# Optimization experiments

Hardware: AMD Instinct MI355X
Metric: run time of the kernel (lower is better)

Reference implementation:

```python
import jax, jax.numpy as jnp
import numpy as np


def setup_inputs() -> dict:
    key = jax.random.key(0)
    k1, k2, k3 = jax.random.split(key, 3)
    B, N, F = 32, 1024, 128
    x = jax.random.normal(k1, (B, N, F), dtype=jnp.float32)
    adj = jax.random.uniform(k2, (B, N, N), dtype=jnp.float32)
    # Linear(in_feature=128, out_feature=128) params (Kaiming-ish scale)
    W = jax.random.normal(k3, (F, F), dtype=jnp.float32) * (1.0 / np.sqrt(F))
    b = jnp.zeros((F,), dtype=jnp.float32)
    return {"x": x, "adj": adj, "W": W, "b": b}


def reference(x, adj, W, b):
    # h = W(x) ; dropout is identity in inference mode
    h = jnp.einsum("bnf,fg->bng", x, W) + b          # [B,N,F]
    h = jnp.einsum("bnm,bmf->bnf", adj, h)           # neighbor aggregation
    return jax.nn.relu(h + x)                          # residual + ReLU
```

## Files before the change

kernel.cpp:

```cpp
#include <hip/hip_runtime.h>
#include <stdint.h>

typedef unsigned short u16;
typedef __attribute__((ext_vector_type(4))) u16    u16x4;
typedef __attribute__((ext_vector_type(8))) u16    u16x8;
typedef __attribute__((ext_vector_type(4))) float  f32x4;
typedef __attribute__((ext_vector_type(8))) __bf16 bf16x8;

__device__ __forceinline__ u16 f2bf(float f) {
    union { float f; uint32_t u; } v; v.f = f;
    uint32_t u = v.u;
    uint32_t rb = 0x7FFFu + ((u >> 16) & 1u);
    return (u16)((u + rb) >> 16);
}

__device__ __forceinline__ bf16x8 cvt8(f32x4 a, f32x4 b) {
    bf16x8 r;
    r[0] = (__bf16)a.x; r[1] = (__bf16)a.y; r[2] = (__bf16)a.z; r[3] = (__bf16)a.w;
    r[4] = (__bf16)b.x; r[5] = (__bf16)b.y; r[6] = (__bf16)b.z; r[7] = (__bf16)b.w;
    return r;
}

__global__ __launch_bounds__(256) void gcn_wt(const float* __restrict__ W,
                                              u16* __restrict__ Wt) {
    int idx = blockIdx.x * 256 + threadIdx.x;
    int k = idx >> 7, f = idx & 127;
    Wt[f * 128 + k] = f2bf(W[idx]);
}

__global__ __launch_bounds__(256) void gcn_xw(const float* __restrict__ x,
                                              const u16* __restrict__ Wt,
                                              const float* __restrict__ bias,
                                              u16* __restrict__ hT) {
    __shared__ u16 Wl[128 * 128];
    __shared__ u16 Xl[128 * 128];
    const int t  = threadIdx.x;
    const int bb = blockIdx.x >> 3;
    const int n0 = (blockIdx.x & 7) << 7;

#pragma unroll
    for (int i = 0; i < 16; ++i) {
        int o  = i * 256 + t;
        int f  = o >> 5;
        int kb = (o & 31) * 8;
        u16x4 v = *(const u16x4*)((const char*)Wt + o * 8);
        *(u16x4*)((char*)Wl + f * 256 + (kb ^ ((f & 7) << 4))) = v;
    }
    const float* xb = x + (size_t)bb * (1024 * 128) + (size_t)n0 * 128;
#pragma unroll
    for (int i = 0; i < 16; ++i) {
        int o4 = i * 256 + t;
        int n  = o4 >> 5;
        int kb = (o4 & 31) * 8;
        f32x4 v = *(const f32x4*)(xb + (size_t)o4 * 4);
        u16x4 h; h.x = f2bf(v.x); h.y = f2bf(v.y); h.z = f2bf(v.z); h.w = f2bf(v.w);
        *(u16x4*)((char*)Xl + n * 256 + (kb ^ ((n & 7) << 4))) = h;
    }
    __syncthreads();

    const int w = t >> 6, l = t & 63;
    const int wr = w >> 1, wc = w & 1;
    f32x4 acc[4][4] = {};
#pragma unroll
    for (int kk = 0; kk < 4; ++kk) {
        const int kbyte = kk * 64 + (l >> 4) * 16;
        bf16x8 a[4], b[4];
#pragma unroll
        for (int mf = 0; mf < 4; ++mf) {
            int fl = wr * 64 + mf * 16 + (l & 15);
            a[mf] = *(const bf16x8*)((const char*)Wl + fl * 256 + (kbyte ^ ((fl & 7) << 4)));
        }
#pragma unroll
        for (int nn = 0; nn < 4; ++nn) {
            int nl = wc * 64 + nn * 16 + (l & 15);
            b[nn] = *(const bf16x8*)((const char*)Xl + nl * 256 + (kbyte ^ ((nl & 7) << 4)));
        }
#pragma unroll
        for (int mf = 0; mf < 4; ++mf)
#pragma unroll
            for (int nn = 0; nn < 4; ++nn)
                acc[mf][nn] = __builtin_amdgcn_mfma_f32_16x16x32_bf16(
                    a[mf], b[nn], acc[mf][nn], 0, 0, 0);
    }

    u16* ho = hT + (size_t)bb * 131072;
#pragma unroll
    for (int mf = 0; mf < 4; ++mf) {
        int fbase = wr * 64 + mf * 16 + (l >> 4) * 4;
#pragma unroll
        for (int r = 0; r < 4; ++r) {
            float bv = bias[fbase + r];
#pragma unroll
            for (int nn = 0; nn < 4; ++nn) {
                int n = wc * 64 + nn * 16 + (l & 15);
                ho[(size_t)(fbase + r) * 1024 + n0 + n] = f2bf(acc[mf][nn][r] + bv);
            }
        }
    }
}

__global__ __launch_bounds__(256) void gcn_agg(const float* __restrict__ adj,
                                               const u16* __restrict__ hT,
                                               const float* __restrict__ x,
                                               float* __restrict__ out) {
    __shared__ float Al[2][64 * 64];
    __shared__ u16   Bl[2][128 * 64];

    const int t = threadIdx.x;
    const int L  = (blockIdx.x & 7) * 64 + (blockIdx.x >> 3);
    const int bb = L >> 4;
    const int r0 = (L & 15) << 6;

    const float* adjb = adj + (size_t)bb * 1048576 + (size_t)r0 * 1024;
    const u16*   hTb  = hT + (size_t)bb * 131072;

    const int w = t >> 6, l = t & 63;
    const int wr = w >> 1, wc = w & 1;

    const float* srcA[4];
    const u16*   srcB[4];
#pragma unroll
    for (int i = 0; i < 4; ++i) {
        int c  = (w * 4 + i) * 64 + l;
        int rA = c >> 4, cbA = ((c & 15) * 16) ^ ((rA & 7) << 4);
        srcA[i] = adjb + (size_t)rA * 1024 + (cbA >> 2);
        int fB = c >> 3, cbB = ((c & 7) * 16) ^ ((fB & 7) << 4);
        srcB[i] = hTb + (size_t)fB * 1024 + (cbB >> 1);
    }

#define STAGE(buf, ks)                                                          \
    do {                                                                        \
        const int k0 = (ks) * 64;                                               \
        _Pragma("unroll")                                                       \
        for (int i = 0; i < 4; ++i) {                                           \
            __builtin_amdgcn_global_load_lds(                                   \
                (const __attribute__((address_space(1))) void*)(srcA[i] + k0),  \
                (__attribute__((address_space(3))) void*)((char*)&Al[buf][0] + (w * 4 + i) * 1024), \
                16, 0, 0);                                                      \
            __builtin_amdgcn_global_load_lds(                                   \
                (const __attribute__((address_space(1))) void*)(srcB[i] + k0),  \
                (__attribute__((address_space(3))) void*)((char*)&Bl[buf][0] + (w * 4 + i) * 1024), \
                16, 0, 0);                                                      \
        }                                                                       \
    } while (0)

#define COMPUTE(buf)                                                            \
    do {                                                                        \
        _Pragma("unroll")                                                       \
        for (int kk = 0; kk < 2; ++kk) {                                        \
            const int ke = kk * 32 + (l >> 4) * 8;                              \
            bf16x8 a[2], b[4];                                                  \
            _Pragma("unroll")                                                   \
            for (int mf = 0; mf < 2; ++mf) {                                    \
                int rl  = wr * 32 + mf * 16 + (l & 15);                         \
                int cb0 = (ke * 4) ^ ((rl & 7) << 4);                           \
                int cb1 = (ke * 4 + 16) ^ ((rl & 7) << 4);                      \
                f32x4 lo = *(const f32x4*)((const char*)&Al[buf][0] + rl * 256 + cb0); \
                f32x4 hi = *(const f32x4*)((const char*)&Al[buf][0] + rl * 256 + cb1); \
                a[mf] = cvt8(lo, hi);                                           \
            }                                                                   \
            _Pragma("unroll")                                                   \
            for (int nn = 0; nn < 4; ++nn) {                                    \
                int fl = wc * 64 + nn * 16 + (l & 15);                          \
                int cb = (ke * 2) ^ ((fl & 7) << 4);                            \
                b[nn] = *(const bf16x8*)((const char*)&Bl[buf][0] + fl * 128 + cb); \
            }                                                                   \
            _Pragma("unroll")                                                   \
            for (int mf = 0; mf < 2; ++mf)                                      \
                _Pragma("unroll")                                               \
                for (int nn = 0; nn < 4; ++nn)                                  \
                    acc[mf][nn] = __builtin_amdgcn_mfma_f32_16x16x32_bf16(      \
                        a[mf], b[nn], acc[mf][nn], 0, 0, 0);                    \
        }                                                                       \
    } while (0)

    f32x4 acc[2][4] = {};

    STAGE(0, 0);
    __syncthreads();
    for (int ks = 0; ks < 16; ks += 2) {
        STAGE(1, ks + 1);
        COMPUTE(0);
        __syncthreads();
        if (ks + 2 < 16) STAGE(0, ks + 2);
        COMPUTE(1);
        __syncthreads();
    }
#undef STAGE
#undef COMPUTE

    const float* xb = x + (size_t)bb * 131072;
    float*       ob = out + (size_t)bb * 131072;
#pragma unroll
    for (int mf = 0; mf < 2; ++mf) {
#pragma unroll
        for (int j = 0; j < 4; ++j) {
            int r = r0 + wr * 32 + mf * 16 + (l >> 4) * 4 + j;
#pragma unroll
            for (int nn = 0; nn < 4; ++nn) {
                int f = wc * 64 + nn * 16 + (l & 15);
                size_t idx = (size_t)r * 128 + f;
                float v = acc[mf][nn][j] + xb[idx];
                ob[idx] = fmaxf(v, 0.0f);
            }
        }
    }
}

extern "C" void kernel_launch(void* const* d_in, const int* in_sizes, int n_in,
                              void* d_out, int out_size, void* d_ws, size_t ws_size,
                              hipStream_t stream) {
    const float* x    = (const float*)d_in[0];
    const float* adj  = (const float*)d_in[1];
    const float* W    = (const float*)d_in[2];
    const float* bias = (const float*)d_in[3];
    float* out = (float*)d_out;

    u16* hT = (u16*)d_ws;
    u16* Wt = (u16*)((char*)d_ws + (size_t)32 * 131072 * 2);

    gcn_wt <<<dim3(64),  dim3(256), 0, stream>>>(W, Wt);
    gcn_xw <<<dim3(256), dim3(256), 0, stream>>>(x, Wt, bias, hT);
    gcn_agg<<<dim3(512), dim3(256), 0, stream>>>(adj, hT, x, out);
}
```

Measured before the change: 44.96 us.

## Stage adjacency through registers, convert to bf16 before LDS, use 512-thread blocks

The aggregation kernel no longer uses direct global-to-LDS async loads. Each thread now loads fp32 adj and bf16 hT into registers two k-steps ahead, converts adj to bf16 once, and writes it into a swizzled bf16 LDS tile. This halves LDS footprint and LDS read traffic for A and removes the repeated per-wave fp32-to-bf16 conversion. Blocks grow to 512 threads (8 waves, 16 rows each) with a custom waitcnt+barrier. The trade-off is more register pressure, manual rounding work per thread, and extra VGPR-to-LDS write instructions.

```diff
diff --git a/kernel.cpp b/kernel.cpp
--- a/kernel.cpp
+++ b/kernel.cpp
@@ -12,13 +12,6 @@
     uint32_t u = v.u;
     uint32_t rb = 0x7FFFu + ((u >> 16) & 1u);
     return (u16)((u + rb) >> 16);
-}
-
-__device__ __forceinline__ bf16x8 cvt8(f32x4 a, f32x4 b) {
-    bf16x8 r;
-    r[0] = (__bf16)a.x; r[1] = (__bf16)a.y; r[2] = (__bf16)a.z; r[3] = (__bf16)a.w;
-    r[4] = (__bf16)b.x; r[5] = (__bf16)b.y; r[6] = (__bf16)b.z; r[7] = (__bf16)b.w;
-    return r;
 }
 
 __global__ __launch_bounds__(256) void gcn_wt(const float* __restrict__ W,
@@ -99,12 +92,12 @@
     }
 }
 
-__global__ __launch_bounds__(256) void gcn_agg(const float* __restrict__ adj,
-                                               const u16* __restrict__ hT,
-                                               const float* __restrict__ x,
-                                               float* __restrict__ out) {
-    __shared__ float Al[2][64 * 64];
-    __shared__ u16   Bl[2][128 * 64];
+__global__ __launch_bounds__(512, 4) void gcn_agg(const float* __restrict__ adj,
+                                                  const u16* __restrict__ hT,
+                                                  const float* __restrict__ x,
+                                                  float* __restrict__ out) {
+    __shared__ u16 Al[2][64 * 64];
+    __shared__ u16 Bl[2][128 * 64];
 
     const int t = threadIdx.x;
     const int L  = (blockIdx.x & 7) * 64 + (blockIdx.x >> 3);
@@ -117,92 +110,92 @@
     const int w = t >> 6, l = t & 63;
     const int wr = w >> 1, wc = w & 1;
 
-    const float* srcA[4];
-    const u16*   srcB[4];
-#pragma unroll
-    for (int i = 0; i < 4; ++i) {
-        int c  = (w * 4 + i) * 64 + l;
-        int rA = c >> 4, cbA = ((c & 15) * 16) ^ ((rA & 7) << 4);
-        srcA[i] = adjb + (size_t)rA * 1024 + (cbA >> 2);
-        int fB = c >> 3, cbB = ((c & 7) * 16) ^ ((fB & 7) << 4);
-        srcB[i] = hTb + (size_t)fB * 1024 + (cbB >> 1);
-    }
-
-#define STAGE(buf, ks)                                                          \
-    do {                                                                        \
-        const int k0 = (ks) * 64;                                               \
-        _Pragma("unroll")                                                       \
-        for (int i = 0; i < 4; ++i) {                                           \
-            __builtin_amdgcn_global_load_lds(                                   \
-                (const __attribute__((address_space(1))) void*)(srcA[i] + k0),  \
-                (__attribute__((address_space(3))) void*)((char*)&Al[buf][0] + (w * 4 + i) * 1024), \
-                16, 0, 0);                                                      \
-            __builtin_amdgcn_global_load_lds(                                   \
-                (const __attribute__((address_space(1))) void*)(srcB[i] + k0),  \
-                (__attribute__((address_space(3))) void*)((char*)&Bl[buf][0] + (w * 4 + i) * 1024), \
-                16, 0, 0);                                                      \
-        }                                                                       \
+    const int rA  = t >> 3, k8 = t & 7;
+    const float* gA  = adjb + (size_t)rA * 1024 + k8 * 8;
+    const u16*   gB0 = hTb + (size_t)rA * 1024 + k8 * 8;
+    const u16*   gB1 = gB0 + 64 * 1024;
+    const int ldsA  = rA * 128 + ((k8 * 16) ^ ((rA & 7) << 4));
+    const int ldsB0 = rA * 128 + ((k8 * 16) ^ ((rA & 7) << 4));
+    const int ldsB1 = (64 + rA) * 128 + ((k8 * 16) ^ ((rA & 7) << 4));
+
+#define LOADT(ar, br, ks)                                   \
+    do {                                                    \
+        const int k0 = (ks) * 64;                           \
+        ar[0] = *(const f32x4*)(gA + k0);                   \
+        ar[1] = *(const f32x4*)(gA + k0 + 4);               \
+        br[0] = *(const u16x8*)(gB0 + k0);                  \
+        br[1] = *(const u16x8*)(gB1 + k0);                  \
     } while (0)
+
+#define WRITET(buf, ar, br)                                 \
+    do {                                                    \
+        u16x8 ha;                                           \
+        ha[0] = f2bf(ar[0].x); ha[1] = f2bf(ar[0].y);       \
+        ha[2] = f2bf(ar[0].z); ha[3] = f2bf(ar[0].w);       \
+        ha[4] = f2bf(ar[1].x); ha[5] = f2bf(ar[1].y);       \
+        ha[6] = f2bf(ar[1].z); ha[7] = f2bf(ar[1].w);       \
+        *(u16x8*)((char*)&Al[buf][0] + ldsA)  = ha;         \
+        *(u16x8*)((char*)&Bl[buf][0] + ldsB0) = br[0];      \
+        *(u16x8*)((char*)&Bl[buf][0] + ldsB1) = br[1];      \
+    } while (0)
+
+#define BARRIER() asm volatile("s_waitcnt lgkmcnt(0)\ns_barrier" ::: "memory")
 
 #define COMPUTE(buf)                                                            \
     do {                                                                        \
         _Pragma("unroll")                                                       \
         for (int kk = 0; kk < 2; ++kk) {                                        \
-            const int ke = kk * 32 + (l >> 4) * 8;                              \
-            bf16x8 a[2], b[4];                                                  \
-            _Pragma("unroll")                                                   \
-            for (int mf = 0; mf < 2; ++mf) {                                    \
-                int rl  = wr * 32 + mf * 16 + (l & 15);                         \
-                int cb0 = (ke * 4) ^ ((rl & 7) << 4);                           \
-                int cb1 = (ke * 4 + 16) ^ ((rl & 7) << 4);                      \
-                f32x4 lo = *(const f32x4*)((const char*)&Al[buf][0] + rl * 256 + cb0); \
-                f32x4 hi = *(const f32x4*)((const char*)&Al[buf][0] + rl * 256 + cb1); \
-                a[mf] = cvt8(lo, hi);                                           \
-            }                                                                   \
+            const int kbyte = kk * 64 + (l >> 4) * 16;                          \
+            const int rl = wr * 16 + (l & 15);                                  \
+            bf16x8 a = *(const bf16x8*)((const char*)&Al[buf][0] + rl * 128 +   \
+                                        (kbyte ^ ((rl & 7) << 4)));             \
+            bf16x8 b[4];                                                        \
             _Pragma("unroll")                                                   \
             for (int nn = 0; nn < 4; ++nn) {                                    \
                 int fl = wc * 64 + nn * 16 + (l & 15);                          \
-                int cb = (ke * 2) ^ ((fl & 7) << 4);                            \
-                b[nn] = *(const bf16x8*)((const char*)&Bl[buf][0] + fl * 128 + cb); \
+                b[nn] = *(const bf16x8*)((const char*)&Bl[buf][0] + fl * 128 +  \
+                                         (kbyte ^ ((fl & 7) << 4)));            \
             }                                                                   \
             _Pragma("unroll")                                                   \
-            for (int mf = 0; mf < 2; ++mf)                                      \
-                _Pragma("unroll")                                               \
-                for (int nn = 0; nn < 4; ++nn)                                  \
-                    acc[mf][nn] = __builtin_amdgcn_mfma_f32_16x16x32_bf16(      \
-                        a[mf], b[nn], acc[mf][nn], 0, 0, 0);                    \
+            for (int nn = 0; nn < 4; ++nn)                                      \
+                acc[nn] = __builtin_amdgcn_mfma_f32_16x16x32_bf16(              \
+                    a, b[nn], acc[nn], 0, 0, 0);                                \
         }                                                                       \
     } while (0)
 
-    f32x4 acc[2][4] = {};
-
-    STAGE(0, 0);
-    __syncthreads();
+    f32x4 acc[4] = {};
+    f32x4 a0[2], a1[2];
+    u16x8 b0[2], b1[2];
+
+    LOADT(a0, b0, 0);
+    LOADT(a1, b1, 1);
+#pragma unroll
     for (int ks = 0; ks < 16; ks += 2) {
-        STAGE(1, ks + 1);
+        WRITET(0, a0, b0);
+        BARRIER();
+        if (ks + 2 < 16) LOADT(a0, b0, ks + 2);
         COMPUTE(0);
-        __syncthreads();
-        if (ks + 2 < 16) STAGE(0, ks + 2);
+        WRITET(1, a1, b1);
+        BARRIER();
+        if (ks + 3 < 16) LOADT(a1, b1, ks + 3);
         COMPUTE(1);
-        __syncthreads();
-    }
-#undef STAGE
+    }
+#undef LOADT
+#undef WRITET
+#undef BARRIER
 #undef COMPUTE
 
     const float* xb = x + (size_t)bb * 131072;
     float*       ob = out + (size_t)bb * 131072;
 #pragma unroll
-    for (int mf = 0; mf < 2; ++mf) {
-#pragma unroll
-        for (int j = 0; j < 4; ++j) {
-            int r = r0 + wr * 32 + mf * 16 + (l >> 4) * 4 + j;
-#pragma unroll
-            for (int nn = 0; nn < 4; ++nn) {
-                int f = wc * 64 + nn * 16 + (l & 15);
-                size_t idx = (size_t)r * 128 + f;
-                float v = acc[mf][nn][j] + xb[idx];
-                ob[idx] = fmaxf(v, 0.0f);
-            }
+    for (int j = 0; j < 4; ++j) {
+        int r = r0 + wr * 16 + (l >> 4) * 4 + j;
+#pragma unroll
+        for (int nn = 0; nn < 4; ++nn) {
+            int f = wc * 64 + nn * 16 + (l & 15);
+            size_t idx = (size_t)r * 128 + f;
+            float v = acc[nn][j] + xb[idx];
+            ob[idx] = fmaxf(v, 0.0f);
         }
     }
 }
@@ -221,5 +214,5 @@
 
     gcn_wt <<<dim3(64),  dim3(256), 0, stream>>>(W, Wt);
     gcn_xw <<<dim3(256), dim3(256), 0, stream>>>(x, Wt, bias, hT);
-    gcn_agg<<<dim3(512), dim3(256), 0, stream>>>(adj, hT, x, out);
-}
+    gcn_agg<<<dim3(512), dim3(512), 0, stream>>>(adj, hT, x, out);
+}
```

Result: faster. 40.89 us (-9.0%).
